# Kernel tuning notes

Hardware: AMD Instinct MI355X
Metric: run time of the kernel (lower is better)

Reference implementation:

```python
import jax, jax.numpy as jnp
import numpy as np

N_NODES = 100000
N_EDGES = 1600000


def setup_inputs() -> dict:
    key = jax.random.key(0)
    k1, k2, k3, k4, k5, k6 = jax.random.split(key, 6)
    x = jax.random.normal(k1, (N_NODES, 2), dtype=jnp.float32)
    edge_index = jax.random.randint(k2, (2, N_EDGES), 0, N_NODES, dtype=jnp.int64)
    # Glorot-style init for GCN weights, zeros for biases (PyG defaults)
    W1 = jax.random.normal(k3, (2, 64), dtype=jnp.float32) * (1.0 / np.sqrt(2.0))
    b1 = jnp.zeros((64,), dtype=jnp.float32)
    W2 = jax.random.normal(k4, (64, 1), dtype=jnp.float32) * (1.0 / np.sqrt(64.0))
    b2 = jnp.zeros((1,), dtype=jnp.float32)
    return {"x": x, "edge_index": edge_index, "W1": W1, "b1": b1, "W2": W2, "b2": b2}


def reference(x, edge_index, W1, b1, W2, b2):
    N = x.shape[0]
    row, col = edge_index[0], edge_index[1]  # source, target (PyG flow source_to_target)
    # symmetric GCN normalization, degrees from target index (no self loops)
    deg = jax.ops.segment_sum(jnp.ones(edge_index.shape[1], x.dtype), col, num_segments=N)
    deg_inv_sqrt = jnp.where(deg > 0, jnp.where(deg > 0, deg, 1.0) ** -0.5, 0.0)
    norm = (deg_inv_sqrt[row] * deg_inv_sqrt[col])[:, None]  # [E,1]

    def gcn_conv(h, W, b):
        h = h @ W                       # [N,F_out] tiny GEMM
        msg = h[row] * norm             # gather + scale: [E,F_out]
        agg = jax.ops.segment_sum(msg, col, num_segments=N)  # scatter-add
        return agg + b

    h = jax.nn.relu(gcn_conv(x, W1, b1))   # dropout is identity in eval mode
    out = jax.nn.relu(gcn_conv(h, W2, b2))
    return out
```

## Files before the change

### kernel.cpp

```cpp
#include <hip/hip_runtime.h>
#include <math.h>

#define NN 100000
#define NE 1600000
#define BKT 448
#define NB 224
#define EPB 6400
#define NPB 250
#define STRIDE 8192
#define RT 1024

__global__ void __launch_bounds__(RT) reorder_kernel(
        const int* __restrict__ row, const int* __restrict__ col,
        unsigned* __restrict__ cursor, unsigned* __restrict__ packed) {
    __shared__ int h[NB], lb[NB];
    __shared__ unsigned gaddr[NB], glim[NB];
    __shared__ int wsum[RT / 64];
    __shared__ uint2 sga[EPB];
    const int t = threadIdx.x;
    const int lane = t & 63, wid = t >> 6;
    const int e0 = blockIdx.x * EPB;

    for (int i = t; i < NB; i += RT) h[i] = 0;
    __syncthreads();

    const int4* rv = (const int4*)(row + e0);
    const int4* cv = (const int4*)(col + e0);
    unsigned pk[8]; int bb[8];
#pragma unroll
    for (int u = 0; u < 8; ++u) bb[u] = -1;
#pragma unroll
    for (int g = 0; g < 2; ++g) {
        int grp = g * RT + t;
        if (grp < EPB / 4) {
            int4 r4 = rv[grp], c4 = cv[grp];
            int rr[4] = {r4.x, r4.y, r4.z, r4.w};
            int cc[4] = {c4.x, c4.y, c4.z, c4.w};
#pragma unroll
            for (int j = 0; j < 4; ++j) {
                int b = cc[j] / BKT;
                int cl = cc[j] - b * BKT;
                pk[4 * g + j] = ((unsigned)rr[j] << 9) | (unsigned)cl;
                bb[4 * g + j] = b;
            }
        }
    }
#pragma unroll
    for (int u = 0; u < 8; ++u)
        if (bb[u] >= 0) atomicAdd(&h[bb[u]], 1);
    __syncthreads();

    int v = (t < NB) ? h[t] : 0;
    int incl = v;
#pragma unroll
    for (int d = 1; d < 64; d <<= 1) {
        int u2 = __shfl_up(incl, d);
        if (lane >= d) incl += u2;
    }
    if (lane == 63) wsum[wid] = incl;
    __syncthreads();
    int off = 0;
#pragma unroll
    for (int j = 0; j < 3; ++j)
        if (j < wid) off += wsum[j];
    if (t < NB) {
        lb[t] = off + incl - v;
        unsigned base = v ? atomicAdd(&cursor[t], (unsigned)v) : 0u;
        gaddr[t] = (unsigned)t * STRIDE + base;
        glim[t]  = (unsigned)(t + 1) * STRIDE;
    }
    __syncthreads();
    for (int i = t; i < NB; i += RT) h[i] = 0;
    __syncthreads();

#pragma unroll
    for (int u = 0; u < 8; ++u) {
        if (bb[u] >= 0) {
            int b = bb[u];
            int r = atomicAdd(&h[b], 1);
            unsigned a = gaddr[b] + (unsigned)r;
            if (a >= glim[b]) a = 0xFFFFFFFFu;
            sga[lb[b] + r] = make_uint2(pk[u], a);
        }
    }
    __syncthreads();
    for (int i = t; i < EPB; i += RT) {
        uint2 e = sga[i];
        if (e.y != 0xFFFFFFFFu) packed[e.y] = e.x;
    }
}

__global__ void __launch_bounds__(RT) degree_kernel(
        const unsigned* __restrict__ packed, const unsigned* __restrict__ cursor,
        const float2* __restrict__ x2,
        float* __restrict__ dis, float2* __restrict__ y2) {
    __shared__ int cnt[BKT];
    const int t = threadIdx.x;
    const int b = blockIdx.x;
    const unsigned s0 = (unsigned)b * STRIDE;
    const int L = min((int)cursor[b], STRIDE);
    const int L4 = L >> 2;

    for (int i = t; i < BKT; i += RT) cnt[i] = 0;
    __syncthreads();

    const uint4* pv4 = (const uint4*)(packed + s0);
    for (int g = t; g < L4; g += RT) {
        uint4 p4 = pv4[g];
        atomicAdd(&cnt[p4.x & 511u], 1);
        atomicAdd(&cnt[p4.y & 511u], 1);
        atomicAdd(&cnt[p4.z & 511u], 1);
        atomicAdd(&cnt[p4.w & 511u], 1);
    }
    for (int i = 4 * L4 + t; i < L; i += RT)
        atomicAdd(&cnt[packed[s0 + i] & 511u], 1);
    __syncthreads();

    int node = b * BKT + t;
    if (t < BKT && node < NN) {
        int v = cnt[t];
        float dv = (v > 0) ? rsqrtf((float)v) : 0.0f;
        dis[node] = dv;
        float2 xv = x2[node];
        y2[node] = make_float2(xv.x * dv, xv.y * dv);
    }
}

__global__ void __launch_bounds__(RT) sortconv1_kernel(
        const unsigned* __restrict__ packed, const unsigned* __restrict__ cursor,
        const float2* __restrict__ y2,
        const float* __restrict__ W1, const float* __restrict__ b1,
        const float* __restrict__ W2,
        unsigned* __restrict__ srow, int2* __restrict__ node_rng,
        float* __restrict__ z2) {
    __shared__ int cnt[BKT], rk[BKT], sexA[BKT];
    __shared__ int wsum[(BKT + 63) / 64];
    __shared__ float sW0[64], sW1[64], sb1[64], sW2[64];
    __shared__ unsigned srt[STRIDE];
    const int t = threadIdx.x;
    const int lane = t & 63, wid = t >> 6;
    const int b = blockIdx.x;
    const unsigned s0 = (unsigned)b * STRIDE;
    const int L = min((int)cursor[b], STRIDE);
    const int L4 = L >> 2;

    if (t < 64) { sW0[t] = W1[t]; sW1[t] = W1[64 + t]; sb1[t] = b1[t]; sW2[t] = W2[t]; }
    for (int i = t; i < BKT; i += RT) { cnt[i] = 0; rk[i] = 0; }
    __syncthreads();

    const uint4* pv4 = (const uint4*)(packed + s0);
    for (int g = t; g < L4; g += RT) {
        uint4 p4 = pv4[g];
        atomicAdd(&cnt[p4.x & 511u], 1);
        atomicAdd(&cnt[p4.y & 511u], 1);
        atomicAdd(&cnt[p4.z & 511u], 1);
        atomicAdd(&cnt[p4.w & 511u], 1);
    }
    for (int i = 4 * L4 + t; i < L; i += RT)
        atomicAdd(&cnt[packed[s0 + i] & 511u], 1);
    __syncthreads();

    int v = (t < BKT) ? cnt[t] : 0;
    int incl = v;
#pragma unroll
    for (int d = 1; d < 64; d <<= 1) {
        int u2 = __shfl_up(incl, d);
        if (lane >= d) incl += u2;
    }
    if (lane == 63 && wid < (BKT + 63) / 64) wsum[wid] = incl;
    __syncthreads();
    int off = 0;
#pragma unroll
    for (int j = 0; j < (BKT + 63) / 64 - 1; ++j)
        if (j < wid) off += wsum[j];
    if (t < BKT) {
        int sex = off + incl - v;
        sexA[t] = sex;
        int node = b * BKT + t;
        if (node < NN)
            node_rng[node] = make_int2((int)(s0 + sex), (int)(s0 + sex + v));
    }
    __syncthreads();

    for (int g = t; g < L4; g += RT) {
        uint4 p4 = pv4[g];
        unsigned pp[4] = {p4.x, p4.y, p4.z, p4.w};
#pragma unroll
        for (int j = 0; j < 4; ++j) {
            int cl = pp[j] & 511u;
            int r = atomicAdd(&rk[cl], 1);
            srt[sexA[cl] + r] = pp[j] >> 9;
        }
    }
    for (int i = 4 * L4 + t; i < L; i += RT) {
        unsigned p = packed[s0 + i];
        int cl = p & 511u;
        int r = atomicAdd(&rk[cl], 1);
        srt[sexA[cl] + r] = p >> 9;
    }
    __syncthreads();

    uint4* so4 = (uint4*)(srow + s0);
    for (int g = t; g < L4; g += RT) so4[g] = ((const uint4*)srt)[g];
    for (int i = 4 * L4 + t; i < L; i += RT) srow[s0 + i] = srt[i];

    const int tau = t >> 1, par = t & 1;
    if (t < 2 * BKT) {
        int start = sexA[tau], deg = cnt[tau];
        float sx = 0.f, sy = 0.f;
        for (int k = start + par; k < start + deg; k += 2) {
            float2 w = y2[srt[k]];
            sx += w.x; sy += w.y;
        }
        sx += __shfl_xor(sx, 1); sy += __shfl_xor(sy, 1);
        float dv = (deg > 0) ? rsqrtf((float)deg) : 0.0f;
        float a0 = sx * dv, a1 = sy * dv;
        float acc = 0.0f;
        int j0 = par * 32;
#pragma unroll
        for (int jj = 0; jj < 32; ++jj) {
            int j = j0 + jj;
            float h = fmaf(a0, sW0[j], fmaf(a1, sW1[j], sb1[j]));
            acc = fmaf(fmaxf(h, 0.0f), sW2[j], acc);
        }
        acc += __shfl_xor(acc, 1);
        int node = b * BKT + tau;
        if (par == 0 && node < NN) z2[node] = acc * dv;
    }
}

__global__ void conv2_kernel(const unsigned* __restrict__ srow, const int2* __restrict__ node_rng,
                             const float* __restrict__ z2, const float* __restrict__ dis,
                             const float* __restrict__ b2, float* __restrict__ out) {
    int t = threadIdx.x;
    int lane = t & 3;
    int node = blockIdx.x * 64 + (t >> 2);
    if (node >= NN) return;
    int2 rng = node_rng[node];
    float s = 0.f;
    for (int k = rng.x + lane; k < rng.y; k += 4)
        s += z2[srow[k]];
    s += __shfl_xor(s, 1);
    s += __shfl_xor(s, 2);
    if (lane == 0)
        out[node] = fmaxf(fmaf(dis[node], s, b2[0]), 0.0f);
}

extern "C" void kernel_launch(void* const* d_in, const int* in_sizes, int n_in,
                              void* d_out, int out_size, void* d_ws, size_t ws_size,
                              hipStream_t stream) {
    const float* x  = (const float*)d_in[0];
    const int*   ei = (const int*)d_in[1];
    const float* W1 = (const float*)d_in[2];
    const float* b1 = (const float*)d_in[3];
    const float* W2 = (const float*)d_in[4];
    const float* b2 = (const float*)d_in[5];
    float* out = (float*)d_out;

    const int* row = ei;
    const int* col = ei + NE;

    unsigned* packed   = (unsigned*)d_ws;
    unsigned* srow     = packed + (size_t)NB * STRIDE;
    float2*   y2       = (float2*)(srow + (size_t)NB * STRIDE);
    float*    dis      = (float*)(y2 + NN);
    float*    z2       = dis + NN;
    int2*     node_rng = (int2*)(z2 + NN);
    unsigned* cursor   = (unsigned*)(node_rng + NN);

    hipMemsetAsync(cursor, 0, NB * sizeof(unsigned), stream);

    reorder_kernel  <<<NPB, RT, 0, stream>>>(row, col, cursor, packed);
    degree_kernel   <<<NB, RT, 0, stream>>>(packed, cursor, (const float2*)x, dis, y2);
    sortconv1_kernel<<<NB, RT, 0, stream>>>(packed, cursor, (const float2*)y2,
                                            W1, b1, W2, srow, node_rng, z2);
    conv2_kernel    <<<(NN + 63) / 64, 256, 0, stream>>>(srow, node_rng, z2, dis, b2, out);
}
```

Baseline: 111.3 us.

## Move bucket scan into degree kernel and pack node ranges into 32 bits

```diff
diff --git a/kernel.cpp b/kernel.cpp
--- a/kernel.cpp
+++ b/kernel.cpp
@@ -3,11 +3,11 @@
 
 #define NN 100000
 #define NE 1600000
-#define BKT 448
-#define NB 224
+#define BKT 391
+#define NB 256
 #define EPB 6400
 #define NPB 250
-#define STRIDE 8192
+#define STRIDE 7168
 #define RT 1024
 
 __global__ void __launch_bounds__(RT) reorder_kernel(
@@ -90,12 +90,14 @@
     }
 }
 
-__global__ void __launch_bounds__(RT) degree_kernel(
+__global__ void __launch_bounds__(RT) degscan_kernel(
         const unsigned* __restrict__ packed, const unsigned* __restrict__ cursor,
         const float2* __restrict__ x2,
-        float* __restrict__ dis, float2* __restrict__ y2) {
+        float2* __restrict__ y2, unsigned* __restrict__ rng32) {
     __shared__ int cnt[BKT];
+    __shared__ int wsum[(BKT + 63) / 64];
     const int t = threadIdx.x;
+    const int lane = t & 63, wid = t >> 6;
     const int b = blockIdx.x;
     const unsigned s0 = (unsigned)b * STRIDE;
     const int L = min((int)cursor[b], STRIDE);
@@ -116,72 +118,57 @@
         atomicAdd(&cnt[packed[s0 + i] & 511u], 1);
     __syncthreads();
 
-    int node = b * BKT + t;
-    if (t < BKT && node < NN) {
-        int v = cnt[t];
-        float dv = (v > 0) ? rsqrtf((float)v) : 0.0f;
-        dis[node] = dv;
-        float2 xv = x2[node];
-        y2[node] = make_float2(xv.x * dv, xv.y * dv);
+    int v = (t < BKT) ? cnt[t] : 0;
+    int incl = v;
+#pragma unroll
+    for (int d = 1; d < 64; d <<= 1) {
+        int u2 = __shfl_up(incl, d);
+        if (lane >= d) incl += u2;
+    }
+    if (lane == 63 && wid < (BKT + 63) / 64) wsum[wid] = incl;
+    __syncthreads();
+    int off = 0;
+#pragma unroll
+    for (int j = 0; j < (BKT + 63) / 64 - 1; ++j)
+        if (j < wid) off += wsum[j];
+    if (t < BKT) {
+        int sex = off + incl - v;
+        int node = b * BKT + t;
+        if (node < NN) {
+            float dv = (v > 0) ? rsqrtf((float)v) : 0.0f;
+            float2 xv = x2[node];
+            y2[node] = make_float2(xv.x * dv, xv.y * dv);
+            rng32[node] = ((unsigned)sex << 16) | (unsigned)v;
+        }
     }
 }
 
 __global__ void __launch_bounds__(RT) sortconv1_kernel(
         const unsigned* __restrict__ packed, const unsigned* __restrict__ cursor,
-        const float2* __restrict__ y2,
+        const float2* __restrict__ y2, const unsigned* __restrict__ rng32,
         const float* __restrict__ W1, const float* __restrict__ b1,
         const float* __restrict__ W2,
-        unsigned* __restrict__ srow, int2* __restrict__ node_rng,
-        float* __restrict__ z2) {
-    __shared__ int cnt[BKT], rk[BKT], sexA[BKT];
-    __shared__ int wsum[(BKT + 63) / 64];
+        unsigned* __restrict__ srow, float* __restrict__ z2) {
+    __shared__ int rk[BKT], sexA[BKT], cntA[BKT];
     __shared__ float sW0[64], sW1[64], sb1[64], sW2[64];
     __shared__ unsigned srt[STRIDE];
     const int t = threadIdx.x;
-    const int lane = t & 63, wid = t >> 6;
     const int b = blockIdx.x;
     const unsigned s0 = (unsigned)b * STRIDE;
     const int L = min((int)cursor[b], STRIDE);
     const int L4 = L >> 2;
 
     if (t < 64) { sW0[t] = W1[t]; sW1[t] = W1[64 + t]; sb1[t] = b1[t]; sW2[t] = W2[t]; }
-    for (int i = t; i < BKT; i += RT) { cnt[i] = 0; rk[i] = 0; }
+    for (int i = t; i < BKT; i += RT) rk[i] = 0;
+    if (t < BKT) {
+        int node = b * BKT + t;
+        unsigned u = (node < NN) ? rng32[node] : 0u;
+        sexA[t] = (int)(u >> 16);
+        cntA[t] = (int)(u & 0xFFFFu);
+    }
     __syncthreads();
 
     const uint4* pv4 = (const uint4*)(packed + s0);
-    for (int g = t; g < L4; g += RT) {
-        uint4 p4 = pv4[g];
-        atomicAdd(&cnt[p4.x & 511u], 1);
-        atomicAdd(&cnt[p4.y & 511u], 1);
-        atomicAdd(&cnt[p4.z & 511u], 1);
-        atomicAdd(&cnt[p4.w & 511u], 1);
-    }
-    for (int i = 4 * L4 + t; i < L; i += RT)
-        atomicAdd(&cnt[packed[s0 + i] & 511u], 1);
-    __syncthreads();
-
-    int v = (t < BKT) ? cnt[t] : 0;
-    int incl = v;
-#pragma unroll
-    for (int d = 1; d < 64; d <<= 1) {
-        int u2 = __shfl_up(incl, d);
-        if (lane >= d) incl += u2;
-    }
-    if (lane == 63 && wid < (BKT + 63) / 64) wsum[wid] = incl;
-    __syncthreads();
-    int off = 0;
-#pragma unroll
-    for (int j = 0; j < (BKT + 63) / 64 - 1; ++j)
-        if (j < wid) off += wsum[j];
-    if (t < BKT) {
-        int sex = off + incl - v;
-        sexA[t] = sex;
-        int node = b * BKT + t;
-        if (node < NN)
-            node_rng[node] = make_int2((int)(s0 + sex), (int)(s0 + sex + v));
-    }
-    __syncthreads();
-
     for (int g = t; g < L4; g += RT) {
         uint4 p4 = pv4[g];
         unsigned pp[4] = {p4.x, p4.y, p4.z, p4.w};
@@ -206,7 +193,7 @@
 
     const int tau = t >> 1, par = t & 1;
     if (t < 2 * BKT) {
-        int start = sexA[tau], deg = cnt[tau];
+        int start = sexA[tau], deg = cntA[tau];
         float sx = 0.f, sy = 0.f;
         for (int k = start + par; k < start + deg; k += 2) {
             float2 w = y2[srt[k]];
@@ -229,21 +216,26 @@
     }
 }
 
-__global__ void conv2_kernel(const unsigned* __restrict__ srow, const int2* __restrict__ node_rng,
-                             const float* __restrict__ z2, const float* __restrict__ dis,
+__global__ void conv2_kernel(const unsigned* __restrict__ srow, const unsigned* __restrict__ rng32,
+                             const float* __restrict__ z2,
                              const float* __restrict__ b2, float* __restrict__ out) {
     int t = threadIdx.x;
     int lane = t & 3;
     int node = blockIdx.x * 64 + (t >> 2);
     if (node >= NN) return;
-    int2 rng = node_rng[node];
+    unsigned u = rng32[node];
+    int bk = node / BKT;
+    unsigned start = (unsigned)bk * STRIDE + (u >> 16);
+    int deg = (int)(u & 0xFFFFu);
     float s = 0.f;
-    for (int k = rng.x + lane; k < rng.y; k += 4)
+    for (unsigned k = start + lane; k < start + (unsigned)deg; k += 4)
         s += z2[srow[k]];
     s += __shfl_xor(s, 1);
     s += __shfl_xor(s, 2);
-    if (lane == 0)
-        out[node] = fmaxf(fmaf(dis[node], s, b2[0]), 0.0f);
+    if (lane == 0) {
+        float dv = (deg > 0) ? rsqrtf((float)deg) : 0.0f;
+        out[node] = fmaxf(fmaf(dv, s, b2[0]), 0.0f);
+    }
 }
 
 extern "C" void kernel_launch(void* const* d_in, const int* in_sizes, int n_in,
@@ -260,19 +252,18 @@
     const int* row = ei;
     const int* col = ei + NE;
 
-    unsigned* packed   = (unsigned*)d_ws;
-    unsigned* srow     = packed + (size_t)NB * STRIDE;
-    float2*   y2       = (float2*)(srow + (size_t)NB * STRIDE);
-    float*    dis      = (float*)(y2 + NN);
-    float*    z2       = dis + NN;
-    int2*     node_rng = (int2*)(z2 + NN);
-    unsigned* cursor   = (unsigned*)(node_rng + NN);
+    unsigned* packed = (unsigned*)d_ws;
+    unsigned* srow   = packed + (size_t)NB * STRIDE;
+    float2*   y2     = (float2*)(srow + (size_t)NB * STRIDE);
+    float*    z2     = (float*)(y2 + NN);
+    unsigned* rng32  = (unsigned*)(z2 + NN);
+    unsigned* cursor = rng32 + NN;
 
     hipMemsetAsync(cursor, 0, NB * sizeof(unsigned), stream);
 
     reorder_kernel  <<<NPB, RT, 0, stream>>>(row, col, cursor, packed);
-    degree_kernel   <<<NB, RT, 0, stream>>>(packed, cursor, (const float2*)x, dis, y2);
-    sortconv1_kernel<<<NB, RT, 0, stream>>>(packed, cursor, (const float2*)y2,
-                                            W1, b1, W2, srow, node_rng, z2);
-    conv2_kernel    <<<(NN + 63) / 64, 256, 0, stream>>>(srow, node_rng, z2, dis, b2, out);
-}
+    degscan_kernel  <<<NB, RT, 0, stream>>>(packed, cursor, (const float2*)x, y2, rng32);
+    sortconv1_kernel<<<NB, RT, 0, stream>>>(packed, cursor, (const float2*)y2, rng32,
+                                            W1, b1, W2, srow, z2);
+    conv2_kernel    <<<(NN + 63) / 64, 256, 0, stream>>>(srow, rng32, z2, b2, out);
+}
```

Measured after the change: 110.2 us. About the same (-1.0%).
